# Performance work log

Measured on AMD Instinct MI355X. Metric: run time of the kernel, lower is better.

Reference implementation:

```python
import jax, jax.numpy as jnp
import numpy as np
import math

DEPTH = 12
LAMBDA_INIT = 0.8 - 0.6 * math.exp(-0.3 * DEPTH)
EPS = 1e-5


def setup_inputs() -> dict:
    key = jax.random.key(0)
    ks = jax.random.split(key, 10)
    B, S, E, H, D = 2, 2048, 1024, 8, 64
    query = jax.random.normal(ks[0], (B, S, E), dtype=jnp.float32)
    init = 0.02
    Wq = jax.random.normal(ks[1], (E, 2 * H * D), dtype=jnp.float32) * init
    Wk = jax.random.normal(ks[2], (E, 2 * H * D), dtype=jnp.float32) * init
    Wv = jax.random.normal(ks[3], (E, 2 * H * D), dtype=jnp.float32) * init
    Wo = jax.random.normal(ks[4], (2 * H * D, E), dtype=jnp.float32) * init
    lq1 = jax.random.normal(ks[5], (D,), dtype=jnp.float32) * 0.1
    lk1 = jax.random.normal(ks[6], (D,), dtype=jnp.float32) * 0.1
    lq2 = jax.random.normal(ks[7], (D,), dtype=jnp.float32) * 0.1
    lk2 = jax.random.normal(ks[8], (D,), dtype=jnp.float32) * 0.1
    subln_w = jnp.ones((2 * D,), dtype=jnp.float32)
    return {"query": query, "Wq": Wq, "Wk": Wk, "Wv": Wv, "Wo": Wo,
            "lq1": lq1, "lk1": lk1, "lq2": lq2, "lk2": lk2, "subln_w": subln_w}


def reference(query, Wq, Wk, Wv, Wo, lq1, lk1, lq2, lk2, subln_w):
    B, S, E = query.shape
    D = lq1.shape[0]
    H = Wq.shape[1] // (2 * D)
    scaling = D ** -0.5
    # projections -> (B, 2H, S, D) for q/k, (B, H, S, 2D) for v
    q = (query @ Wq).reshape(B, S, 2 * H, D).transpose(0, 2, 1, 3) * scaling
    k = (query @ Wk).reshape(B, S, 2 * H, D).transpose(0, 2, 1, 3)
    v = (query @ Wv).reshape(B, S, H, 2 * D).transpose(0, 2, 1, 3)
    score = jnp.einsum('bhqd,bhkd->bhqk', q, k)  # (B, 2H, S, S)
    score = jnp.nan_to_num(score)
    score = jax.nn.softmax(score.astype(jnp.float32), axis=-1).astype(score.dtype)
    lambda_1 = jnp.exp(jnp.sum(lq1 * lk1))
    lambda_2 = jnp.exp(jnp.sum(lq2 * lk2))
    lambda_full = lambda_1 - lambda_2 + LAMBDA_INIT
    score = score.reshape(B, H, 2, S, S)
    score = score[:, :, 0] - lambda_full * score[:, :, 1]  # (B, H, S, S)
    attn = jnp.einsum('bhqk,bhkd->bhqd', score, v)  # (B, H, S, 2D)
    # RMSNorm over last dim (computed in fp32, cast back), affine weight
    af = attn.astype(jnp.float32)
    attn = (af * jax.lax.rsqrt(jnp.mean(af * af, axis=-1, keepdims=True) + EPS)).astype(attn.dtype)
    attn = attn * subln_w
    attn = attn * (1.0 - LAMBDA_INIT)
    attn = attn.transpose(0, 2, 1, 3).reshape(B, S, H * 2 * D)
    return attn @ Wo
```

## Files before the change

kernel.cpp:

```cpp
#include <hip/hip_runtime.h>

typedef __attribute__((ext_vector_type(4))) float f32x4;
typedef __attribute__((ext_vector_type(8))) short bf16x8;
typedef unsigned short u16;
typedef unsigned int u32;

#define LAMBDA_INIT 0.7836057665311429f
#define ONE_MINUS_LI 0.2163942334688571f
#define QSCALE_LOG2 0.1803368801111137f

__device__ __forceinline__ u16 f2b(float f){
  union { float f; unsigned u; } v; v.f = f;
  unsigned r = v.u + 0x7fff + ((v.u >> 16) & 1);
  return (u16)(r >> 16);
}

__device__ __forceinline__ f32x4 mfma16(bf16x8 a, bf16x8 b, f32x4 c){
  return __builtin_amdgcn_mfma_f32_16x16x32_bf16(a, b, c, 0, 0, 0);
}

__device__ __forceinline__ float exp2_raw(float x){
  float r;
  asm("v_exp_f32 %0, %1" : "=v"(r) : "v"(x));
  return r;
}

__device__ __forceinline__ void async16(void* lds, const void* g){
  __builtin_amdgcn_global_load_lds((const __attribute__((address_space(1))) void*)g,
                                   (__attribute__((address_space(3))) void*)lds, 16, 0, 0);
}

__global__ void cvt_kernel(const float4* __restrict__ in, ushort4* __restrict__ out, int n4){
  int i = blockIdx.x * blockDim.x + threadIdx.x;
  if (i < n4){
    float4 f = in[i];
    ushort4 o; o.x = f2b(f.x); o.y = f2b(f.y); o.z = f2b(f.z); o.w = f2b(f.w);
    out[i] = o;
  }
}

__global__ void wtrans(const float* __restrict__ Wq, const float* __restrict__ Wk,
                       const float* __restrict__ Wv, const float* __restrict__ Wo,
                       u16* __restrict__ Wqkvt, u16* __restrict__ Wot){
  __shared__ float t[32][33];
  int z = blockIdx.z;
  const float* in = (z == 0) ? Wq : (z == 1) ? Wk : (z == 2) ? Wv : Wo;
  u16* out = (z < 3) ? (Wqkvt + (size_t)z * 1048576) : Wot;
  int c0 = blockIdx.x * 32, r0 = blockIdx.y * 32;
  int tx = threadIdx.x, ty = threadIdx.y;
  for (int i = 0; i < 32; i += 8) t[ty + i][tx] = in[(size_t)(r0 + ty + i) * 1024 + c0 + tx];
  __syncthreads();
  for (int i = 0; i < 32; i += 8) out[(size_t)(c0 + ty + i) * 1024 + r0 + tx] = f2b(t[tx][ty + i]);
}

template<int PERM>
__global__ void transpose_bf16(const u16* __restrict__ in, u16* __restrict__ out, int R, int C){
  __shared__ u16 t[32][34];
  int c0 = blockIdx.x * 32, r0 = blockIdx.y * 32;
  size_t boff = (size_t)blockIdx.z * R * C;
  int tx = threadIdx.x, ty = threadIdx.y;
  for (int i = 0; i < 32; i += 8) t[ty + i][tx] = in[boff + (size_t)(r0 + ty + i) * C + c0 + tx];
  __syncthreads();
  for (int i = 0; i < 32; i += 8){
    int dv = c0 + ty + i, s = r0 + tx;
    int sx;
    if (PERM){
      int sl = s & 63;
      int n = sl >> 4, g = (sl >> 2) & 3, r = sl & 3;
      int pos = (s & ~63) | ((n >> 1) << 5) | (g << 3) | ((n & 1) << 2) | r;
      sx = (pos & ~63) | ((((pos >> 3) & 7) ^ (dv & 7)) << 3) | (pos & 7);
    } else sx = s;
    out[boff + (size_t)dv * R + sx] = t[tx][ty + i];
  }
}

template<int BN, int EPI>
__global__ __launch_bounds__(256, 2) void gemm_async(
    const u16* __restrict__ A, const u16* __restrict__ Bt, float* __restrict__ Cp,
    u16* __restrict__ Qo, u16* __restrict__ Ko, u16* __restrict__ Vo,
    int M, int N, int K, int gm){
  constexpr int BCH = BN / 32;
  __shared__ u16 As[2][128 * 64];
  __shared__ u16 Bs[2][BN * 64];
  int tid = threadIdx.x, w = tid >> 6, lane = tid & 63;
  int l16 = lane & 15, grp = lane >> 4;
  int wr = w >> 1, wc = w & 1;
  int nwg = gridDim.x, bid = blockIdx.x;
  int idx = (bid & 7) * (nwg >> 3) + (bid >> 3);
  int m0 = (idx & (gm - 1)) * 128, n0 = (idx / gm) * BN;

  int sr = lane >> 3;
  int sc = ((lane & 7) ^ sr) << 3;
  const u16* pA = A  + (size_t)(m0 + w * 8 + sr) * K + sc;
  const u16* pB = Bt + (size_t)(n0 + w * 8 + sr) * K + sc;

  f32x4 acc[4][BN / 32] = {};

#define STAGEG(bb, k0) do{                                             \
    _Pragma("unroll")                                                  \
    for (int i = 0; i < 4; i++)                                        \
      async16(&As[bb][i * 2048 + w * 512], pA + (k0) + (size_t)i * 32 * K); \
    _Pragma("unroll")                                                  \
    for (int i = 0; i < BCH; i++)                                      \
      async16(&Bs[bb][i * 2048 + w * 512], pB + (k0) + (size_t)i * 32 * K); \
  } while(0)

  STAGEG(0, 0);
  int niter = K >> 6;
  for (int kt = 0; kt < niter; kt++){
    int cur = kt & 1;
    if (kt < niter - 1){
      STAGEG(cur ^ 1, (kt + 1) << 6);
      if constexpr (BN == 128) asm volatile("s_waitcnt vmcnt(8)" ::: "memory");
      else                     asm volatile("s_waitcnt vmcnt(6)" ::: "memory");
    } else {
      asm volatile("s_waitcnt vmcnt(0)" ::: "memory");
    }
    __builtin_amdgcn_s_barrier();

    const u16* Ap = As[cur];
    const u16* Bp = Bs[cur];
    #pragma unroll
    for (int kk = 0; kk < 2; kk++){
      bf16x8 a[4], b[BN / 32];
      #pragma unroll
      for (int m = 0; m < 4; m++){
        int r = wr * 64 + m * 16 + l16;
        a[m] = *(const bf16x8*)&Ap[r * 64 + (((kk * 4 + grp) ^ (r & 7)) << 3)];
      }
      #pragma unroll
      for (int n = 0; n < BCH; n++){
        int r = wc * (BN / 2) + n * 16 + l16;
        b[n] = *(const bf16x8*)&Bp[r * 64 + (((kk * 4 + grp) ^ (r & 7)) << 3)];
      }
      #pragma unroll
      for (int m = 0; m < 4; m++)
        #pragma unroll
        for (int n = 0; n < BCH; n++)
          acc[m][n] = mfma16(a[m], b[n], acc[m][n]);
    }
    if (kt < niter - 1){
      asm volatile("s_waitcnt lgkmcnt(0)" ::: "memory");
      __builtin_amdgcn_s_barrier();
    }
  }
#undef STAGEG

  if constexpr (EPI == 0){
    #pragma unroll
    for (int m = 0; m < 4; m++)
      #pragma unroll
      for (int n = 0; n < BCH; n++)
        #pragma unroll
        for (int r = 0; r < 4; r++)
          Cp[(size_t)(m0 + wr * 64 + m * 16 + grp * 4 + r) * N + n0 + wc * (BN / 2) + n * 16 + l16]
            = acc[m][n][r];
  } else {
    int proj = n0 >> 10;
    #pragma unroll
    for (int m = 0; m < 4; m++){
      int row = m0 + wr * 64 + m * 16 + grp * 4;
      #pragma unroll
      for (int n = 0; n < BCH; n++){
        int col = n0 + wc * (BN / 2) + n * 16 + l16;
        int cn = col & 1023;
        if (proj == 0){
          #pragma unroll
          for (int r = 0; r < 4; r++)
            Qo[(size_t)(row + r) * 1024 + cn] = f2b(acc[m][n][r] * QSCALE_LOG2);
        } else if (proj == 1){
          #pragma unroll
          for (int r = 0; r < 4; r++){
            int cs = (cn & ~63) | ((((cn >> 3) & 7) ^ ((row + r) & 7)) << 3) | (cn & 7);
            Ko[(size_t)(row + r) * 1024 + cs] = f2b(acc[m][n][r]);
          }
        } else {
          #pragma unroll
          for (int r = 0; r < 4; r++)
            Vo[(size_t)(row + r) * 1024 + cn] = f2b(acc[m][n][r]);
        }
      }
    }
  }
}

__global__ __launch_bounds__(256, 2) void diff_attn(
    const u16* __restrict__ Qb, const u16* __restrict__ Kb, const u16* __restrict__ Vt,
    const float* __restrict__ lq1, const float* __restrict__ lk1,
    const float* __restrict__ lq2, const float* __restrict__ lk2,
    const float* __restrict__ slw, u16* __restrict__ attnb){
  __shared__ u16 Ksh[2][2][64 * 64];
  __shared__ u16 Vsh[2][128 * 64];
  __shared__ float lam_s;

  int tid = threadIdx.x, w = tid >> 6, lane = tid & 63;
  int l16 = lane & 15, grp = lane >> 4;
  int bid = blockIdx.x;
  int h = bid & 7, qt = (bid >> 3) & 31, b = bid >> 8;
  int tb = b * 2048 + qt * 64;

  if (tid < 64){
    float p1 = lq1[tid] * lk1[tid], p2 = lq2[tid] * lk2[tid];
    #pragma unroll
    for (int m = 32; m >= 1; m >>= 1){ p1 += __shfl_xor(p1, m); p2 += __shfl_xor(p2, m); }
    if (tid == 0) lam_s = __expf(p1) - __expf(p2) + LAMBDA_INIT;
  }

  const u16* gK1 = Kb + (size_t)(b * 2048 + w * 16 + (lane >> 3)) * 1024 + 128 * h + (lane & 7) * 8;
  const u16* gK2 = gK1 + 64;
  const u16* gV  = Vt + (size_t)(b * 1024 + 128 * h + w * 32 + (lane >> 3)) * 2048 + (lane & 7) * 8;

  bf16x8 q1[2], q2[2];
  {
    const u16* qr = Qb + (size_t)(tb + w * 16 + l16) * 1024 + 128 * h;
    q1[0] = *(const bf16x8*)(qr + grp * 8);
    q1[1] = *(const bf16x8*)(qr + 32 + grp * 8);
    q2[0] = *(const bf16x8*)(qr + 64 + grp * 8);
    q2[1] = *(const bf16x8*)(qr + 96 + grp * 8);
  }

  bf16x8 ones;
  #pragma unroll
  for (int i = 0; i < 8; i++) ones[i] = (short)0x3F80;

#define STAGE(bb, PK1, PK2, PV) do{                         \
    async16(&Ksh[bb][0][w * 1024],       (PK1));            \
    async16(&Ksh[bb][0][w * 1024 + 512], (PK1) + 8192);     \
    async16(&Ksh[bb][1][w * 1024],       (PK2));            \
    async16(&Ksh[bb][1][w * 1024 + 512], (PK2) + 8192);     \
    async16(&Vsh[bb][w * 2048],          (PV));             \
    async16(&Vsh[bb][w * 2048 + 512],    (PV) + 16384);     \
    async16(&Vsh[bb][w * 2048 + 1024],   (PV) + 32768);     \
    async16(&Vsh[bb][w * 2048 + 1536],   (PV) + 49152);     \
  } while(0)

  STAGE(0, gK1, gK2, gV);
  gK1 += 65536; gK2 += 65536; gV += 64;
  __syncthreads();

  int xo0 = ((grp ^ (l16 & 7)) << 3);
  int xo1 = (((4 + grp) ^ (l16 & 7)) << 3);

  f32x4 O1[9] = {}, O2[9] = {};

  for (int kt = 0; kt < 32; kt++){
    int cur = kt & 1;
    if (kt < 31){
      STAGE(cur ^ 1, gK1, gK2, gV);
      gK1 += 65536; gK2 += 65536; gV += 64;
      asm volatile("s_waitcnt vmcnt(8)" ::: "memory");
    } else {
      asm volatile("s_waitcnt vmcnt(0)" ::: "memory");
    }
    __builtin_amdgcn_s_barrier();

    const u16* K1p = Ksh[cur][0];
    const u16* K2p = Ksh[cur][1];
    const u16* Vp  = Vsh[cur];

    f32x4 s1[4], s2[4];
    #pragma unroll
    for (int n = 0; n < 4; n++){ s1[n] = (f32x4){0,0,0,0}; s2[n] = (f32x4){0,0,0,0}; }
    #pragma unroll
    for (int n = 0; n < 4; n++){
      int rb = (n * 16 + l16) << 6;
      bf16x8 k1a = *(const bf16x8*)&K1p[rb + xo0];
      bf16x8 k1b = *(const bf16x8*)&K1p[rb + xo1];
      bf16x8 k2a = *(const bf16x8*)&K2p[rb + xo0];
      bf16x8 k2b = *(const bf16x8*)&K2p[rb + xo1];
      s1[n] = mfma16(k1a, q1[0], s1[n]);
      s1[n] = mfma16(k1b, q1[1], s1[n]);
      s2[n] = mfma16(k2a, q2[0], s2[n]);
      s2[n] = mfma16(k2b, q2[1], s2[n]);
    }

    bf16x8 pbA[2], pbB[2];
    {
      float p[16];
      #pragma unroll
      for (int n = 0; n < 4; n++)
        #pragma unroll
        for (int r = 0; r < 4; r++) p[n * 4 + r] = exp2_raw(s1[n][r] - 4.0f);
      union { u32 w[4]; bf16x8 v; } u0, u1;
      #pragma unroll
      for (int j = 0; j < 4; j++){
        asm("v_cvt_pk_bf16_f32 %0, %1, %2" : "=v"(u0.w[j]) : "v"(p[2 * j]),     "v"(p[2 * j + 1]));
        asm("v_cvt_pk_bf16_f32 %0, %1, %2" : "=v"(u1.w[j]) : "v"(p[8 + 2 * j]), "v"(p[9 + 2 * j]));
      }
      pbA[0] = u0.v; pbA[1] = u1.v;
    }
    {
      float p[16];
      #pragma unroll
      for (int n = 0; n < 4; n++)
        #pragma unroll
        for (int r = 0; r < 4; r++) p[n * 4 + r] = exp2_raw(s2[n][r] - 4.0f);
      union { u32 w[4]; bf16x8 v; } u0, u1;
      #pragma unroll
      for (int j = 0; j < 4; j++){
        asm("v_cvt_pk_bf16_f32 %0, %1, %2" : "=v"(u0.w[j]) : "v"(p[2 * j]),     "v"(p[2 * j + 1]));
        asm("v_cvt_pk_bf16_f32 %0, %1, %2" : "=v"(u1.w[j]) : "v"(p[8 + 2 * j]), "v"(p[9 + 2 * j]));
      }
      pbB[0] = u0.v; pbB[1] = u1.v;
    }

    #pragma unroll
    for (int kk = 0; kk < 2; kk++){
      int xo = kk ? xo1 : xo0;
      #pragma unroll
      for (int n = 0; n < 8; n++){
        bf16x8 av = *(const bf16x8*)&Vp[((n * 16 + l16) << 6) + xo];
        O1[n] = mfma16(av, pbA[kk], O1[n]);
        O2[n] = mfma16(av, pbB[kk], O2[n]);
      }
      O1[8] = mfma16(ones, pbA[kk], O1[8]);
      O2[8] = mfma16(ones, pbB[kk], O2[8]);
    }

    if (kt < 31){
      asm volatile("s_waitcnt lgkmcnt(0)" ::: "memory");
      __builtin_amdgcn_s_barrier();
    }
  }
#undef STAGE

  float lam = lam_s;
  float i1 = 1.f / O1[8][0], i2 = lam / O2[8][0];
  float x[8][4], ss = 0.f;
  #pragma unroll
  for (int n = 0; n < 8; n++)
    #pragma unroll
    for (int r = 0; r < 4; r++){
      float v = O1[n][r] * i1 - O2[n][r] * i2;
      x[n][r] = v; ss += v * v;
    }
  ss += __shfl_xor(ss, 16);
  ss += __shfl_xor(ss, 32);
  float ri = rsqrtf(ss * (1.f / 128.f) + 1e-5f);
  int row = tb + w * 16 + l16;
  #pragma unroll
  for (int n = 0; n < 8; n++){
    float4 sw = *(const float4*)&slw[n * 16 + grp * 4];
    ushort4 o;
    o.x = f2b(x[n][0] * ri * sw.x * ONE_MINUS_LI);
    o.y = f2b(x[n][1] * ri * sw.y * ONE_MINUS_LI);
    o.z = f2b(x[n][2] * ri * sw.z * ONE_MINUS_LI);
    o.w = f2b(x[n][3] * ri * sw.w * ONE_MINUS_LI);
    *(ushort4*)&attnb[(size_t)row * 1024 + h * 128 + n * 16 + grp * 4] = o;
  }
}

extern "C" void kernel_launch(void* const* d_in, const int* in_sizes, int n_in,
                              void* d_out, int out_size, void* d_ws, size_t ws_size,
                              hipStream_t stream){
  const float* query = (const float*)d_in[0];
  const float* Wq = (const float*)d_in[1];
  const float* Wk = (const float*)d_in[2];
  const float* Wv = (const float*)d_in[3];
  const float* Wo = (const float*)d_in[4];
  const float* lq1 = (const float*)d_in[5];
  const float* lk1 = (const float*)d_in[6];
  const float* lq2 = (const float*)d_in[7];
  const float* lk2 = (const float*)d_in[8];
  const float* slw = (const float*)d_in[9];

  char* ws = (char*)d_ws;
  u16* Xbf   = (u16*)(ws + 0);
  u16* Wqkvt = (u16*)(ws + 8388608);
  u16* Wot   = (u16*)(ws + 14680064);
  u16* Qbuf  = (u16*)(ws + 16777216);
  u16* Kbuf  = (u16*)(ws + 25165824);
  u16* Vbuf  = (u16*)(ws + 33554432);
  u16* Vtr   = (u16*)(ws + 41943040);
  u16* Attn  = (u16*)(ws + 50331648);

  cvt_kernel<<<4096, 256, 0, stream>>>((const float4*)query, (ushort4*)Xbf, 1048576);
  wtrans<<<dim3(32, 32, 4), dim3(32, 8), 0, stream>>>(Wq, Wk, Wv, Wo, Wqkvt, Wot);

  gemm_async<128, 1><<<768, 256, 0, stream>>>(Xbf, Wqkvt, nullptr, Qbuf, Kbuf, Vbuf,
                                              4096, 3072, 1024, 32);

  transpose_bf16<1><<<dim3(32, 64, 2), dim3(32, 8), 0, stream>>>(Vbuf, Vtr, 2048, 1024);

  diff_attn<<<512, 256, 0, stream>>>(Qbuf, Kbuf, Vtr, lq1, lk1, lq2, lk2, slw, Attn);

  gemm_async<64, 0><<<512, 256, 0, stream>>>(Attn, Wot, (float*)d_out,
                                             nullptr, nullptr, nullptr,
                                             4096, 1024, 1024, 32);
}
```

Measured before the change: 135.6 us.

## Double query rows per attention block to reuse K/V tiles across two groups

Each wave now handles 32 query rows (two 16-row groups) instead of 16, so every block covers 128 queries and the grid halves to 256 blocks. Each K and V fragment loaded from shared memory feeds MFMAs for both groups, which halves global and LDS traffic for K/V per query. In exchange, register use roughly doubles (launch bounds lowered to 1 block per SM), and 256 blocks on a 256-CU part leaves less occupancy to hide latency.

```diff
diff --git a/kernel.cpp b/kernel.cpp
--- a/kernel.cpp
+++ b/kernel.cpp
@@ -184,7 +184,7 @@
   }
 }
 
-__global__ __launch_bounds__(256, 2) void diff_attn(
+__global__ __launch_bounds__(256, 1) void diff_attn(
     const u16* __restrict__ Qb, const u16* __restrict__ Kb, const u16* __restrict__ Vt,
     const float* __restrict__ lq1, const float* __restrict__ lk1,
     const float* __restrict__ lq2, const float* __restrict__ lk2,
@@ -196,8 +196,8 @@
   int tid = threadIdx.x, w = tid >> 6, lane = tid & 63;
   int l16 = lane & 15, grp = lane >> 4;
   int bid = blockIdx.x;
-  int h = bid & 7, qt = (bid >> 3) & 31, b = bid >> 8;
-  int tb = b * 2048 + qt * 64;
+  int h = bid & 7, qt = (bid >> 3) & 15, b = bid >> 7;
+  int tb = b * 2048 + qt * 128;
 
   if (tid < 64){
     float p1 = lq1[tid] * lk1[tid], p2 = lq2[tid] * lk2[tid];
@@ -210,13 +210,14 @@
   const u16* gK2 = gK1 + 64;
   const u16* gV  = Vt + (size_t)(b * 1024 + 128 * h + w * 32 + (lane >> 3)) * 2048 + (lane & 7) * 8;
 
-  bf16x8 q1[2], q2[2];
-  {
-    const u16* qr = Qb + (size_t)(tb + w * 16 + l16) * 1024 + 128 * h;
-    q1[0] = *(const bf16x8*)(qr + grp * 8);
-    q1[1] = *(const bf16x8*)(qr + 32 + grp * 8);
-    q2[0] = *(const bf16x8*)(qr + 64 + grp * 8);
-    q2[1] = *(const bf16x8*)(qr + 96 + grp * 8);
+  bf16x8 q1[2][2], q2[2][2];
+  #pragma unroll
+  for (int g = 0; g < 2; g++){
+    const u16* qr = Qb + (size_t)(tb + w * 32 + g * 16 + l16) * 1024 + 128 * h;
+    q1[g][0] = *(const bf16x8*)(qr + grp * 8);
+    q1[g][1] = *(const bf16x8*)(qr + 32 + grp * 8);
+    q2[g][0] = *(const bf16x8*)(qr + 64 + grp * 8);
+    q2[g][1] = *(const bf16x8*)(qr + 96 + grp * 8);
   }
 
   bf16x8 ones;
@@ -241,7 +242,7 @@
   int xo0 = ((grp ^ (l16 & 7)) << 3);
   int xo1 = (((4 + grp) ^ (l16 & 7)) << 3);
 
-  f32x4 O1[9] = {}, O2[9] = {};
+  f32x4 O1[2][9] = {}, O2[2][9] = {};
 
   for (int kt = 0; kt < 32; kt++){
     int cur = kt & 1;
@@ -258,50 +259,65 @@
     const u16* K2p = Ksh[cur][1];
     const u16* Vp  = Vsh[cur];
 
-    f32x4 s1[4], s2[4];
-    #pragma unroll
-    for (int n = 0; n < 4; n++){ s1[n] = (f32x4){0,0,0,0}; s2[n] = (f32x4){0,0,0,0}; }
-    #pragma unroll
-    for (int n = 0; n < 4; n++){
-      int rb = (n * 16 + l16) << 6;
-      bf16x8 k1a = *(const bf16x8*)&K1p[rb + xo0];
-      bf16x8 k1b = *(const bf16x8*)&K1p[rb + xo1];
-      bf16x8 k2a = *(const bf16x8*)&K2p[rb + xo0];
-      bf16x8 k2b = *(const bf16x8*)&K2p[rb + xo1];
-      s1[n] = mfma16(k1a, q1[0], s1[n]);
-      s1[n] = mfma16(k1b, q1[1], s1[n]);
-      s2[n] = mfma16(k2a, q2[0], s2[n]);
-      s2[n] = mfma16(k2b, q2[1], s2[n]);
-    }
-
-    bf16x8 pbA[2], pbB[2];
+    bf16x8 pbA[2][2], pbB[2][2];
+
     {
-      float p[16];
-      #pragma unroll
-      for (int n = 0; n < 4; n++)
-        #pragma unroll
-        for (int r = 0; r < 4; r++) p[n * 4 + r] = exp2_raw(s1[n][r] - 4.0f);
-      union { u32 w[4]; bf16x8 v; } u0, u1;
-      #pragma unroll
-      for (int j = 0; j < 4; j++){
-        asm("v_cvt_pk_bf16_f32 %0, %1, %2" : "=v"(u0.w[j]) : "v"(p[2 * j]),     "v"(p[2 * j + 1]));
-        asm("v_cvt_pk_bf16_f32 %0, %1, %2" : "=v"(u1.w[j]) : "v"(p[8 + 2 * j]), "v"(p[9 + 2 * j]));
-      }
-      pbA[0] = u0.v; pbA[1] = u1.v;
+      f32x4 s[2][4] = {};
+      #pragma unroll
+      for (int n = 0; n < 4; n++){
+        int rb = (n * 16 + l16) << 6;
+        bf16x8 ka = *(const bf16x8*)&K1p[rb + xo0];
+        bf16x8 kb = *(const bf16x8*)&K1p[rb + xo1];
+        #pragma unroll
+        for (int g = 0; g < 2; g++){
+          s[g][n] = mfma16(ka, q1[g][0], s[g][n]);
+          s[g][n] = mfma16(kb, q1[g][1], s[g][n]);
+        }
+      }
+      #pragma unroll
+      for (int g = 0; g < 2; g++){
+        float p[16];
+        #pragma unroll
+        for (int n = 0; n < 4; n++)
+          #pragma unroll
+          for (int r = 0; r < 4; r++) p[n * 4 + r] = exp2_raw(s[g][n][r] - 4.0f);
+        union { u32 w[4]; bf16x8 v; } u0, u1;
+        #pragma unroll
+        for (int j = 0; j < 4; j++){
+          asm("v_cvt_pk_bf16_f32 %0, %1, %2" : "=v"(u0.w[j]) : "v"(p[2 * j]),     "v"(p[2 * j + 1]));
+          asm("v_cvt_pk_bf16_f32 %0, %1, %2" : "=v"(u1.w[j]) : "v"(p[8 + 2 * j]), "v"(p[9 + 2 * j]));
+        }
+        pbA[g][0] = u0.v; pbA[g][1] = u1.v;
+      }
     }
     {
-      float p[16];
-      #pragma unroll
-      for (int n = 0; n < 4; n++)
-        #pragma unroll
-        for (int r = 0; r < 4; r++) p[n * 4 + r] = exp2_raw(s2[n][r] - 4.0f);
-      union { u32 w[4]; bf16x8 v; } u0, u1;
-      #pragma unroll
-      for (int j = 0; j < 4; j++){
-        asm("v_cvt_pk_bf16_f32 %0, %1, %2" : "=v"(u0.w[j]) : "v"(p[2 * j]),     "v"(p[2 * j + 1]));
-        asm("v_cvt_pk_bf16_f32 %0, %1, %2" : "=v"(u1.w[j]) : "v"(p[8 + 2 * j]), "v"(p[9 + 2 * j]));
-      }
-      pbB[0] = u0.v; pbB[1] = u1.v;
+      f32x4 s[2][4] = {};
+      #pragma unroll
+      for (int n = 0; n < 4; n++){
+        int rb = (n * 16 + l16) << 6;
+        bf16x8 ka = *(const bf16x8*)&K2p[rb + xo0];
+        bf16x8 kb = *(const bf16x8*)&K2p[rb + xo1];
+        #pragma unroll
+        for (int g = 0; g < 2; g++){
+          s[g][n] = mfma16(ka, q2[g][0], s[g][n]);
+          s[g][n] = mfma16(kb, q2[g][1], s[g][n]);
+        }
+      }
+      #pragma unroll
+      for (int g = 0; g < 2; g++){
+        float p[16];
+        #pragma unroll
+        for (int n = 0; n < 4; n++)
+          #pragma unroll
+          for (int r = 0; r < 4; r++) p[n * 4 + r] = exp2_raw(s[g][n][r] - 4.0f);
+        union { u32 w[4]; bf16x8 v; } u0, u1;
+        #pragma unroll
+        for (int j = 0; j < 4; j++){
+          asm("v_cvt_pk_bf16_f32 %0, %1, %2" : "=v"(u0.w[j]) : "v"(p[2 * j]),     "v"(p[2 * j + 1]));
+          asm("v_cvt_pk_bf16_f32 %0, %1, %2" : "=v"(u1.w[j]) : "v"(p[8 + 2 * j]), "v"(p[9 + 2 * j]));
+        }
+        pbB[g][0] = u0.v; pbB[g][1] = u1.v;
+      }
     }
 
     #pragma unroll
@@ -310,11 +326,17 @@
       #pragma unroll
       for (int n = 0; n < 8; n++){
         bf16x8 av = *(const bf16x8*)&Vp[((n * 16 + l16) << 6) + xo];
-        O1[n] = mfma16(av, pbA[kk], O1[n]);
-        O2[n] = mfma16(av, pbB[kk], O2[n]);
-      }
-      O1[8] = mfma16(ones, pbA[kk], O1[8]);
-      O2[8] = mfma16(ones, pbB[kk], O2[8]);
+        #pragma unroll
+        for (int g = 0; g < 2; g++){
+          O1[g][n] = mfma16(av, pbA[g][kk], O1[g][n]);
+          O2[g][n] = mfma16(av, pbB[g][kk], O2[g][n]);
+        }
+      }
+      #pragma unroll
+      for (int g = 0; g < 2; g++){
+        O1[g][8] = mfma16(ones, pbA[g][kk], O1[g][8]);
+        O2[g][8] = mfma16(ones, pbB[g][kk], O2[g][8]);
+      }
     }
 
     if (kt < 31){
@@ -325,28 +347,31 @@
 #undef STAGE
 
   float lam = lam_s;
-  float i1 = 1.f / O1[8][0], i2 = lam / O2[8][0];
-  float x[8][4], ss = 0.f;
   #pragma unroll
-  for (int n = 0; n < 8; n++)
-    #pragma unroll
-    for (int r = 0; r < 4; r++){
-      float v = O1[n][r] * i1 - O2[n][r] * i2;
-      x[n][r] = v; ss += v * v;
-    }
-  ss += __shfl_xor(ss, 16);
-  ss += __shfl_xor(ss, 32);
-  float ri = rsqrtf(ss * (1.f / 128.f) + 1e-5f);
-  int row = tb + w * 16 + l16;
-  #pragma unroll
-  for (int n = 0; n < 8; n++){
-    float4 sw = *(const float4*)&slw[n * 16 + grp * 4];
-    ushort4 o;
-    o.x = f2b(x[n][0] * ri * sw.x * ONE_MINUS_LI);
-    o.y = f2b(x[n][1] * ri * sw.y * ONE_MINUS_LI);
-    o.z = f2b(x[n][2] * ri * sw.z * ONE_MINUS_LI);
-    o.w = f2b(x[n][3] * ri * sw.w * ONE_MINUS_LI);
-    *(ushort4*)&attnb[(size_t)row * 1024 + h * 128 + n * 16 + grp * 4] = o;
+  for (int g = 0; g < 2; g++){
+    float i1 = 1.f / O1[g][8][0], i2 = lam / O2[g][8][0];
+    float x[8][4], ss = 0.f;
+    #pragma unroll
+    for (int n = 0; n < 8; n++)
+      #pragma unroll
+      for (int r = 0; r < 4; r++){
+        float v = O1[g][n][r] * i1 - O2[g][n][r] * i2;
+        x[n][r] = v; ss += v * v;
+      }
+    ss += __shfl_xor(ss, 16);
+    ss += __shfl_xor(ss, 32);
+    float ri = rsqrtf(ss * (1.f / 128.f) + 1e-5f);
+    int row = tb + w * 32 + g * 16 + l16;
+    #pragma unroll
+    for (int n = 0; n < 8; n++){
+      float4 sw = *(const float4*)&slw[n * 16 + grp * 4];
+      ushort4 o;
+      o.x = f2b(x[n][0] * ri * sw.x * ONE_MINUS_LI);
+      o.y = f2b(x[n][1] * ri * sw.y * ONE_MINUS_LI);
+      o.z = f2b(x[n][2] * ri * sw.z * ONE_MINUS_LI);
+      o.w = f2b(x[n][3] * ri * sw.w * ONE_MINUS_LI);
+      *(ushort4*)&attnb[(size_t)row * 1024 + h * 128 + n * 16 + grp * 4] = o;
+    }
   }
 }
 
@@ -382,7 +407,7 @@
 
   transpose_bf16<1><<<dim3(32, 64, 2), dim3(32, 8), 0, stream>>>(Vbuf, Vtr, 2048, 1024);
 
-  diff_attn<<<512, 256, 0, stream>>>(Qbuf, Kbuf, Vtr, lq1, lk1, lq2, lk2, slw, Attn);
+  diff_attn<<<256, 256, 0, stream>>>(Qbuf, Kbuf, Vtr, lq1, lk1, lq2, lk2, slw, Attn);
 
   gemm_async<64, 0><<<512, 256, 0, stream>>>(Attn, Wot, (float*)d_out,
                                              nullptr, nullptr, nullptr,
```

After: 168.3 us. 24.1% more time.

## Software-pipeline QK^T of next tile with exp and PV of current tile

Applied to the files above, without the earlier changes.

Restructures the attention loop so the QK^T MFMAs for tile kt+1 are issued before the exp/pack and PV MFMAs for tile kt. K and V staging are split so K loads run two tiles ahead and V loads are issued after the end-of-iteration barrier. The goal is to hide the exp/convert latency and LDS reads behind matrix work and to deepen the global prefetch. The cost is extra live accumulator registers, which may lower occupancy, and more intricate wait-count logic.

```diff
diff --git a/kernel.cpp b/kernel.cpp
--- a/kernel.cpp
+++ b/kernel.cpp
@@ -223,87 +223,84 @@
   #pragma unroll
   for (int i = 0; i < 8; i++) ones[i] = (short)0x3F80;
 
-#define STAGE(bb, PK1, PK2, PV) do{                         \
+#define STAGE_K(bb, PK1, PK2) do{                           \
     async16(&Ksh[bb][0][w * 1024],       (PK1));            \
     async16(&Ksh[bb][0][w * 1024 + 512], (PK1) + 8192);     \
     async16(&Ksh[bb][1][w * 1024],       (PK2));            \
     async16(&Ksh[bb][1][w * 1024 + 512], (PK2) + 8192);     \
+  } while(0)
+#define STAGE_V(bb, PV) do{                                 \
     async16(&Vsh[bb][w * 2048],          (PV));             \
     async16(&Vsh[bb][w * 2048 + 512],    (PV) + 16384);     \
     async16(&Vsh[bb][w * 2048 + 1024],   (PV) + 32768);     \
     async16(&Vsh[bb][w * 2048 + 1536],   (PV) + 49152);     \
   } while(0)
 
-  STAGE(0, gK1, gK2, gV);
+  int xo0 = ((grp ^ (l16 & 7)) << 3);
+  int xo1 = (((4 + grp) ^ (l16 & 7)) << 3);
+
+#define QKCOMP(bb, S1, S2) do{                                           \
+    const u16* K1p = Ksh[bb][0];                                         \
+    const u16* K2p = Ksh[bb][1];                                         \
+    _Pragma("unroll")                                                    \
+    for (int n = 0; n < 4; n++){ S1[n] = (f32x4){0,0,0,0}; S2[n] = (f32x4){0,0,0,0}; } \
+    _Pragma("unroll")                                                    \
+    for (int n = 0; n < 4; n++){                                         \
+      int rb = (n * 16 + l16) << 6;                                      \
+      bf16x8 k1a = *(const bf16x8*)&K1p[rb + xo0];                       \
+      bf16x8 k1b = *(const bf16x8*)&K1p[rb + xo1];                       \
+      bf16x8 k2a = *(const bf16x8*)&K2p[rb + xo0];                       \
+      bf16x8 k2b = *(const bf16x8*)&K2p[rb + xo1];                       \
+      S1[n] = mfma16(k1a, q1[0], S1[n]);                                 \
+      S1[n] = mfma16(k1b, q1[1], S1[n]);                                 \
+      S2[n] = mfma16(k2a, q2[0], S2[n]);                                 \
+      S2[n] = mfma16(k2b, q2[1], S2[n]);                                 \
+    }                                                                    \
+  } while(0)
+
+#define EXPPACK(S, PB) do{                                               \
+    float p[16];                                                         \
+    _Pragma("unroll")                                                    \
+    for (int n = 0; n < 4; n++)                                          \
+      _Pragma("unroll")                                                  \
+      for (int r = 0; r < 4; r++) p[n * 4 + r] = exp2_raw(S[n][r] - 4.0f); \
+    union { u32 wd[4]; bf16x8 v; } u0, u1;                               \
+    _Pragma("unroll")                                                    \
+    for (int j = 0; j < 4; j++){                                         \
+      asm("v_cvt_pk_bf16_f32 %0, %1, %2" : "=v"(u0.wd[j]) : "v"(p[2 * j]),     "v"(p[2 * j + 1])); \
+      asm("v_cvt_pk_bf16_f32 %0, %1, %2" : "=v"(u1.wd[j]) : "v"(p[8 + 2 * j]), "v"(p[9 + 2 * j])); \
+    }                                                                    \
+    PB[0] = u0.v; PB[1] = u1.v;                                          \
+  } while(0)
+
+  STAGE_K(0, gK1, gK2); STAGE_V(0, gV);
+  gK1 += 65536; gK2 += 65536; gV += 64;
+  STAGE_K(1, gK1, gK2); STAGE_V(1, gV);
   gK1 += 65536; gK2 += 65536; gV += 64;
   __syncthreads();
 
-  int xo0 = ((grp ^ (l16 & 7)) << 3);
-  int xo1 = (((4 + grp) ^ (l16 & 7)) << 3);
+  f32x4 s1c[4], s2c[4], s1n[4], s2n[4];
+  QKCOMP(0, s1c, s2c);
 
   f32x4 O1[9] = {}, O2[9] = {};
 
   for (int kt = 0; kt < 32; kt++){
     int cur = kt & 1;
-    if (kt < 31){
-      STAGE(cur ^ 1, gK1, gK2, gV);
-      gK1 += 65536; gK2 += 65536; gV += 64;
-      asm volatile("s_waitcnt vmcnt(8)" ::: "memory");
+    if (kt < 30){
+      STAGE_K(cur, gK1, gK2);
+      gK1 += 65536; gK2 += 65536;
+      asm volatile("s_waitcnt vmcnt(4)" ::: "memory");
     } else {
       asm volatile("s_waitcnt vmcnt(0)" ::: "memory");
     }
     __builtin_amdgcn_s_barrier();
 
-    const u16* K1p = Ksh[cur][0];
-    const u16* K2p = Ksh[cur][1];
-    const u16* Vp  = Vsh[cur];
-
-    f32x4 s1[4], s2[4];
-    #pragma unroll
-    for (int n = 0; n < 4; n++){ s1[n] = (f32x4){0,0,0,0}; s2[n] = (f32x4){0,0,0,0}; }
-    #pragma unroll
-    for (int n = 0; n < 4; n++){
-      int rb = (n * 16 + l16) << 6;
-      bf16x8 k1a = *(const bf16x8*)&K1p[rb + xo0];
-      bf16x8 k1b = *(const bf16x8*)&K1p[rb + xo1];
-      bf16x8 k2a = *(const bf16x8*)&K2p[rb + xo0];
-      bf16x8 k2b = *(const bf16x8*)&K2p[rb + xo1];
-      s1[n] = mfma16(k1a, q1[0], s1[n]);
-      s1[n] = mfma16(k1b, q1[1], s1[n]);
-      s2[n] = mfma16(k2a, q2[0], s2[n]);
-      s2[n] = mfma16(k2b, q2[1], s2[n]);
-    }
-
+    if (kt < 31) QKCOMP(cur ^ 1, s1n, s2n);
     bf16x8 pbA[2], pbB[2];
-    {
-      float p[16];
-      #pragma unroll
-      for (int n = 0; n < 4; n++)
-        #pragma unroll
-        for (int r = 0; r < 4; r++) p[n * 4 + r] = exp2_raw(s1[n][r] - 4.0f);
-      union { u32 w[4]; bf16x8 v; } u0, u1;
-      #pragma unroll
-      for (int j = 0; j < 4; j++){
-        asm("v_cvt_pk_bf16_f32 %0, %1, %2" : "=v"(u0.w[j]) : "v"(p[2 * j]),     "v"(p[2 * j + 1]));
-        asm("v_cvt_pk_bf16_f32 %0, %1, %2" : "=v"(u1.w[j]) : "v"(p[8 + 2 * j]), "v"(p[9 + 2 * j]));
-      }
-      pbA[0] = u0.v; pbA[1] = u1.v;
-    }
-    {
-      float p[16];
-      #pragma unroll
-      for (int n = 0; n < 4; n++)
-        #pragma unroll
-        for (int r = 0; r < 4; r++) p[n * 4 + r] = exp2_raw(s2[n][r] - 4.0f);
-      union { u32 w[4]; bf16x8 v; } u0, u1;
-      #pragma unroll
-      for (int j = 0; j < 4; j++){
-        asm("v_cvt_pk_bf16_f32 %0, %1, %2" : "=v"(u0.w[j]) : "v"(p[2 * j]),     "v"(p[2 * j + 1]));
-        asm("v_cvt_pk_bf16_f32 %0, %1, %2" : "=v"(u1.w[j]) : "v"(p[8 + 2 * j]), "v"(p[9 + 2 * j]));
-      }
-      pbB[0] = u0.v; pbB[1] = u1.v;
-    }
-
+    EXPPACK(s1c, pbA);
+    EXPPACK(s2c, pbB);
+
+    const u16* Vp = Vsh[cur];
     #pragma unroll
     for (int kk = 0; kk < 2; kk++){
       int xo = kk ? xo1 : xo0;
@@ -320,9 +317,18 @@
     if (kt < 31){
       asm volatile("s_waitcnt lgkmcnt(0)" ::: "memory");
       __builtin_amdgcn_s_barrier();
-    }
-  }
-#undef STAGE
+      if (kt < 30){
+        STAGE_V(cur, gV);
+        gV += 64;
+      }
+      #pragma unroll
+      for (int n = 0; n < 4; n++){ s1c[n] = s1n[n]; s2c[n] = s2n[n]; }
+    }
+  }
+#undef STAGE_K
+#undef STAGE_V
+#undef QKCOMP
+#undef EXPPACK
 
   float lam = lam_s;
   float i1 = 1.f / O1[8][0], i2 = lam / O2[8][0];
```

Measured after the change: 136.0 us. Within noise of the previous version (+0.3%).
